# Kernel tuning notes

Hardware: AMD Instinct MI355X
Metric: run time of the kernel (lower is better)

The kernel has to match this reference:

```python
import jax, jax.numpy as jnp
import numpy as np

VOCAB = 50257
EMBED = 512
HIDDEN = 1024
UNITS = HIDDEN // 2  # per-direction LSTM units
B, S, T = 32, 8, 128


def _lstm_bias(units):
    # Keras unit_forget_bias=True: bias = [0 (i), 1 (f), 0 (c), 0 (o)]
    return jnp.concatenate([jnp.zeros((units,)), jnp.ones((units,)),
                            jnp.zeros((2 * units,))])


def setup_inputs() -> dict:
    key = jax.random.key(0)
    ks = jax.random.split(key, 8)
    # token ids with variable-length zero padding (pad_token_id=0)
    x = jax.random.randint(ks[0], (B, S, T), 1, VOCAB)
    lengths = jax.random.randint(ks[1], (B, S, 1), T // 2, T + 1)
    pos = jnp.arange(T)[None, None, :]
    x = jnp.where(pos < lengths, x, 0).astype(jnp.int32)

    emb_table = jax.random.normal(ks[2], (VOCAB, EMBED), jnp.float32) * 0.05

    def glorot(k, shape):
        fan = np.sqrt(2.0 / (shape[0] + shape[1]))
        return jax.random.normal(k, shape, jnp.float32) * fan

    W_f = glorot(ks[3], (EMBED, 4 * UNITS))
    U_f = glorot(ks[4], (UNITS, 4 * UNITS))
    W_b = glorot(ks[5], (EMBED, 4 * UNITS))
    U_b = glorot(ks[6], (UNITS, 4 * UNITS))
    b_f = _lstm_bias(UNITS)
    b_b = _lstm_bias(UNITS)
    return {"x": x, "emb_table": emb_table,
            "W_f": W_f, "U_f": U_f, "b_f": b_f,
            "W_b": W_b, "U_b": U_b, "b_b": b_b}


def _masked_lstm_final(xW, mask, U):
    """xW: (N, T, 4u) precomputed input projections (+bias); mask: (N, T) bool.
    Returns final hidden state (N, u) with Keras masking semantics: masked
    timesteps are skipped (state held)."""
    N = xW.shape[0]
    u = U.shape[0]
    h0 = jnp.zeros((N, u), xW.dtype)
    c0 = jnp.zeros((N, u), xW.dtype)

    def step(carry, inp):
        h, c = carry
        z, m = inp  # z: (N, 4u), m: (N,)
        z = z + h @ U
        i, f, g, o = jnp.split(z, 4, axis=-1)
        i = jax.nn.sigmoid(i)
        f = jax.nn.sigmoid(f)
        g = jnp.tanh(g)
        o = jax.nn.sigmoid(o)
        c_new = f * c + i * g
        h_new = o * jnp.tanh(c_new)
        m = m[:, None]
        return (jnp.where(m, h_new, h), jnp.where(m, c_new, c)), None

    (hT, _), _ = jax.lax.scan(
        step, (h0, c0),
        (jnp.swapaxes(xW, 0, 1), jnp.swapaxes(mask, 0, 1)))
    return hT


def reference(x, emb_table, W_f, U_f, b_f, W_b, U_b, b_b):
    Bx, Sx, Tx = x.shape
    N = Bx * Sx
    ids = x.reshape(N, Tx)
    mask = ids != 0  # mask_zero=True
    emb = emb_table[ids]  # (N, T, E)

    # forward direction
    xWf = emb @ W_f + b_f  # (N, T, 4u), one big GEMM up front
    h_fwd = _masked_lstm_final(xWf, mask, U_f)

    # backward direction: reverse time and mask (Keras go_backwards)
    emb_rev = emb[:, ::-1, :]
    mask_rev = mask[:, ::-1]
    xWb = emb_rev @ W_b + b_b
    h_bwd = _masked_lstm_final(xWb, mask_rev, U_b)

    out = jnp.concatenate([h_fwd, h_bwd], axis=-1)  # (N, hidden_dim)
    return out.reshape(Bx, Sx, HIDDEN)
```

## Files before the change

kernel.cpp:

```cpp
#include <hip/hip_runtime.h>

typedef _Float16 half_t;
typedef _Float16 half8 __attribute__((ext_vector_type(8)));
typedef float floatx4 __attribute__((ext_vector_type(4)));

#define NSEQ   256
#define TLEN   128
#define EMBD   512
#define UNITSZ 512
#define GC     2048
#define NTOK   32768
#define NCOL   4096
#define KDIM   512

constexpr size_t OFF_EMB = 0;
constexpr size_t OFF_WT  = 33554432;
constexpr size_t OFF_UT  = OFF_WT + 4194304;
constexpr size_t OFF_HB  = OFF_UT + 4194304;
constexpr size_t OFF_CNT = OFF_HB + 1048576;
constexpr size_t OFF_MSK = OFF_CNT + 4096;
constexpr size_t OFF_XW  = OFF_MSK + 4096;

__device__ inline float sigm(float x)  { return 1.0f / (1.0f + __expf(-x)); }
__device__ inline float tanhx(float x) { return 2.0f / (1.0f + __expf(-2.0f * x)) - 1.0f; }

__device__ inline unsigned long long ld8c(const void* p) {
    return __hip_atomic_load((const unsigned long long*)p, __ATOMIC_RELAXED, __HIP_MEMORY_SCOPE_AGENT);
}
__device__ inline void st8c(void* p, unsigned long long v) {
    __hip_atomic_store((unsigned long long*)p, v, __ATOMIC_RELAXED, __HIP_MEMORY_SCOPE_AGENT);
}

__global__ void pack_kernel(const float* __restrict__ Wf, const float* __restrict__ Uf,
                            const float* __restrict__ Wb, const float* __restrict__ Ub,
                            half_t* __restrict__ WT, half_t* __restrict__ UT) {
    int c = blockIdx.x * 256 + threadIdx.x;
    int arr = c >> 18;
    int r = c & 262143;
    int kc = r >> 12;
    int gc = r & 4095;
    int dir = gc >> 11;
    int g = gc & 2047;
    const float* src = (arr == 0) ? (dir ? Wb : Wf) : (dir ? Ub : Uf);
    half_t* dst = (arr == 0) ? WT : UT;
    half8 v;
#pragma unroll
    for (int j = 0; j < 8; ++j)
        v[j] = (half_t)src[(size_t)(kc * 8 + j) * GC + g];
    *(half8*)(dst + (size_t)gc * KDIM + kc * 8) = v;
}

__global__ void zero_kernel(unsigned* __restrict__ hb_and_cnt) {
    int i = blockIdx.x * 256 + threadIdx.x;
    if (i < 263168) hb_and_cnt[i] = 0u;
}

__global__ void mask_kernel(const int* __restrict__ x, unsigned long long* __restrict__ mk) {
    int n = blockIdx.x;
    int l = threadIdx.x;
    unsigned long long b0 = __ballot(x[n * TLEN + l] != 0);
    unsigned long long b1 = __ballot(x[n * TLEN + 64 + l] != 0);
    if (l == 0) { mk[n * 2] = b0; mk[n * 2 + 1] = b1; }
}

__global__ void gather_kernel(const int* __restrict__ x, const float* __restrict__ tab,
                              half_t* __restrict__ embf) {
    int g = blockIdx.x * 256 + threadIdx.x;
    int token = g >> 6;
    int k = (g & 63) * 8;
    int id = x[token];
    const float* s = tab + (size_t)id * EMBD + k;
    float4 a = *(const float4*)(s);
    float4 b = *(const float4*)(s + 4);
    half8 v;
    v[0] = (half_t)a.x; v[1] = (half_t)a.y; v[2] = (half_t)a.z; v[3] = (half_t)a.w;
    v[4] = (half_t)b.x; v[5] = (half_t)b.y; v[6] = (half_t)b.z; v[7] = (half_t)b.w;
    *(half8*)(embf + (size_t)token * EMBD + k) = v;
}

__global__ __launch_bounds__(256, 2) void gemm_kernel(const half_t* __restrict__ embf,
                                                      const half_t* __restrict__ WT,
                                                      const float* __restrict__ bf,
                                                      const float* __restrict__ bb,
                                                      half_t* __restrict__ xw) {
    __shared__ half_t As[128 * 40];
    __shared__ half_t Bs[128 * 40];
    int bx = blockIdx.x;
    int bm = bx & 255, bn = bx >> 8;
    int r0 = bm * 128, c0 = bn * 128;
    int tid = threadIdx.x;
    int w = tid >> 6, l = tid & 63;
    int q = l >> 4, cl = l & 15;
    int mq = (w >> 1) * 64, nq = (w & 1) * 64;

    floatx4 acc[4][4];
#pragma unroll
    for (int a = 0; a < 4; ++a)
#pragma unroll
        for (int b = 0; b < 4; ++b) acc[a][b] = (floatx4){0.f, 0.f, 0.f, 0.f};

    for (int kb = 0; kb < 16; ++kb) {
#pragma unroll
        for (int cc = 0; cc < 2; ++cc) {
            int c = tid + cc * 256;
            int row = c >> 2, qt = c & 3;
            half8 va = *(const half8*)(embf + (size_t)(r0 + row) * KDIM + kb * 32 + qt * 8);
            *(half8*)(As + row * 40 + qt * 8) = va;
            half8 vb = *(const half8*)(WT + (size_t)(c0 + row) * KDIM + kb * 32 + qt * 8);
            *(half8*)(Bs + row * 40 + qt * 8) = vb;
        }
        __syncthreads();
        half8 af[4], bfr[4];
#pragma unroll
        for (int mb = 0; mb < 4; ++mb)
            af[mb] = *(const half8*)(As + (mq + mb * 16 + cl) * 40 + q * 8);
#pragma unroll
        for (int nb = 0; nb < 4; ++nb)
            bfr[nb] = *(const half8*)(Bs + (nq + nb * 16 + cl) * 40 + q * 8);
#pragma unroll
        for (int mb = 0; mb < 4; ++mb)
#pragma unroll
            for (int nb = 0; nb < 4; ++nb)
                acc[mb][nb] = __builtin_amdgcn_mfma_f32_16x16x32_f16(af[mb], bfr[nb], acc[mb][nb], 0, 0, 0);
        __syncthreads();
    }
#pragma unroll
    for (int nb = 0; nb < 4; ++nb) {
        int col = c0 + nq + nb * 16 + cl;
        int dir = col >> 11, gcol = col & 2047;
        float bias = dir ? bb[gcol] : bf[gcol];
#pragma unroll
        for (int mb = 0; mb < 4; ++mb) {
#pragma unroll
            for (int r = 0; r < 4; ++r) {
                int row = r0 + mq + mb * 16 + q * 4 + r;
                xw[(size_t)row * NCOL + col] = (half_t)(acc[mb][nb][r] + bias);
            }
        }
    }
}

__global__ __launch_bounds__(256, 1) void lstm_kernel(const half_t* __restrict__ xw,
                                                      const half_t* __restrict__ UT,
                                                      half_t* __restrict__ hbuf,
                                                      const unsigned long long* __restrict__ mk,
                                                      float* __restrict__ out,
                                                      unsigned* __restrict__ cnt) {
    __shared__ half_t Ast[8192];
    __shared__ half_t Pk[1024];
    int bx = blockIdx.x;
    int dir = bx >> 7;
    int rowg = (bx >> 3) & 15;
    int wgc = bx & 7;
    int tid = threadIdx.x;
    int w = tid >> 6, l = tid & 63;
    int q = l >> 4, cl = l & 15;
    int cg = wgc * 4 + w;
    int ub = cg * 16;
    int ub0 = wgc * 64;
    int r0 = rowg * 16;

    half8 bfrag[64];
#pragma unroll
    for (int kk = 0; kk < 16; ++kk)
#pragma unroll
        for (int cf = 0; cf < 4; ++cf)
            bfrag[kk * 4 + cf] = *(const half8*)(UT + (size_t)(dir * 2048 + cf * 512 + ub + cl) * KDIM + kk * 32 + q * 8);

    unsigned long long mlo[4], mhi[4];
#pragma unroll
    for (int r = 0; r < 4; ++r) {
        int n = r0 + q * 4 + r;
        mlo[r] = mk[n * 2];
        mhi[r] = mk[n * 2 + 1];
    }

    float cs[4] = {0.f, 0.f, 0.f, 0.f};
    float hs[4] = {0.f, 0.f, 0.f, 0.f};
    unsigned* cptr = cnt + (dir * 16 + rowg) * 16;
    int colb = dir * 2048 + ub + cl;

    half_t xv[4][4];
    {
        int tIdx = dir ? 127 : 0;
#pragma unroll
        for (int r = 0; r < 4; ++r) {
            size_t ro = ((size_t)(r0 + q * 4 + r) * TLEN + tIdx) * NCOL;
#pragma unroll
            for (int g = 0; g < 4; ++g)
                xv[g][r] = xw[ro + colb + g * 512];
        }
    }

#pragma unroll 1
    for (int t = 0; t < TLEN; ++t) {
        int tIdx = dir ? (127 - t) : t;
        int rpar = t & 1, wpar = rpar ^ 1;
        if (t > 0) {
            if (tid == 0) {
                while (__hip_atomic_load(cptr, __ATOMIC_RELAXED, __HIP_MEMORY_SCOPE_AGENT) < (unsigned)(32 * t))
                    __builtin_amdgcn_s_sleep(1);
            }
            __syncthreads();
        }
        const half_t* hsrc = hbuf + (size_t)(dir * 2 + rpar) * NSEQ * UNITSZ;
#pragma unroll
        for (int cc = 0; cc < 4; ++cc) {
            int c = tid + cc * 256;
            int kk = c >> 6, ll = c & 63;
            int m = ll & 15, koff = kk * 32 + (ll >> 4) * 8;
            const half_t* sp = hsrc + (size_t)(r0 + m) * UNITSZ + koff;
            union { unsigned long long u[2]; half8 v; } cv;
            cv.u[0] = ld8c(sp);
            cv.u[1] = ld8c(sp + 4);
            *(half8*)(Ast + c * 8) = cv.v;
        }
        __syncthreads();
        floatx4 a0, a1, a2, a3;
#pragma unroll
        for (int r = 0; r < 4; ++r) {
            a0[r] = (float)xv[0][r];
            a1[r] = (float)xv[1][r];
            a2[r] = (float)xv[2][r];
            a3[r] = (float)xv[3][r];
        }
#pragma unroll
        for (int kk = 0; kk < 16; ++kk) {
            half8 af = *(const half8*)(Ast + (kk * 64 + l) * 8);
            a0 = __builtin_amdgcn_mfma_f32_16x16x32_f16(af, bfrag[kk * 4 + 0], a0, 0, 0, 0);
            a1 = __builtin_amdgcn_mfma_f32_16x16x32_f16(af, bfrag[kk * 4 + 1], a1, 0, 0, 0);
            a2 = __builtin_amdgcn_mfma_f32_16x16x32_f16(af, bfrag[kk * 4 + 2], a2, 0, 0, 0);
            a3 = __builtin_amdgcn_mfma_f32_16x16x32_f16(af, bfrag[kk * 4 + 3], a3, 0, 0, 0);
        }
#pragma unroll
        for (int r = 0; r < 4; ++r) {
            unsigned long long mw = (tIdx & 64) ? mhi[r] : mlo[r];
            bool keep = (mw >> (tIdx & 63)) & 1ull;
            float iv = sigm(a0[r]);
            float fv = sigm(a1[r]);
            float gv = tanhx(a2[r]);
            float ov = sigm(a3[r]);
            float cn = fv * cs[r] + iv * gv;
            float hn = ov * tanhx(cn);
            if (keep) { cs[r] = cn; hs[r] = hn; }
            Pk[(q * 4 + r) * 64 + w * 16 + cl] = (half_t)hs[r];
        }
        __syncthreads();
        half_t* hdst = hbuf + (size_t)(dir * 2 + wpar) * NSEQ * UNITSZ;
        {
            int prow = tid >> 4, pch = tid & 15;
            unsigned long long pv = *(const unsigned long long*)(Pk + prow * 64 + pch * 4);
            st8c(hdst + (size_t)(r0 + prow) * UNITSZ + ub0 + pch * 4, pv);
        }
        asm volatile("" ::: "memory");
        if (t + 1 < TLEN) {
            int tN = dir ? (126 - t) : (t + 1);
#pragma unroll
            for (int r = 0; r < 4; ++r) {
                size_t ro = ((size_t)(r0 + q * 4 + r) * TLEN + tN) * NCOL;
#pragma unroll
                for (int g = 0; g < 4; ++g)
                    xv[g][r] = xw[ro + colb + g * 512];
            }
        }
        asm volatile("s_waitcnt vmcnt(16)" ::: "memory");
        if (l == 0)
            __hip_atomic_fetch_add(cptr, 1u, __ATOMIC_RELAXED, __HIP_MEMORY_SCOPE_AGENT);
    }
#pragma unroll
    for (int r = 0; r < 4; ++r) {
        int n = r0 + q * 4 + r;
        out[(size_t)n * 1024 + dir * 512 + ub + cl] = hs[r];
    }
}

extern "C" void kernel_launch(void* const* d_in, const int* in_sizes, int n_in,
                              void* d_out, int out_size, void* d_ws, size_t ws_size,
                              hipStream_t stream) {
    const int*   x    = (const int*)d_in[0];
    const float* tab  = (const float*)d_in[1];
    const float* Wf   = (const float*)d_in[2];
    const float* Uf   = (const float*)d_in[3];
    const float* bf   = (const float*)d_in[4];
    const float* Wb   = (const float*)d_in[5];
    const float* Ub   = (const float*)d_in[6];
    const float* bb   = (const float*)d_in[7];
    float* out = (float*)d_out;

    char* ws = (char*)d_ws;
    half_t*   embf = (half_t*)(ws + OFF_EMB);
    half_t*   WT   = (half_t*)(ws + OFF_WT);
    half_t*   UT   = (half_t*)(ws + OFF_UT);
    half_t*   hbuf = (half_t*)(ws + OFF_HB);
    unsigned* cnt  = (unsigned*)(ws + OFF_CNT);
    unsigned long long* mkb = (unsigned long long*)(ws + OFF_MSK);
    half_t*   xw   = (half_t*)(ws + OFF_XW);
    unsigned* hbz  = (unsigned*)(ws + OFF_HB);

    pack_kernel<<<2048, 256, 0, stream>>>(Wf, Uf, Wb, Ub, WT, UT);
    zero_kernel<<<1028, 256, 0, stream>>>(hbz);
    mask_kernel<<<256, 64, 0, stream>>>(x, mkb);
    gather_kernel<<<8192, 256, 0, stream>>>(x, tab, embf);
    gemm_kernel<<<8192, 256, 0, stream>>>(embf, WT, bf, bb, xw);
    lstm_kernel<<<256, 256, 0, stream>>>(xw, UT, hbuf, mkb, out, cnt);
}
```

Measured before the change: 1.108 ms.

## Interleave two 8-row LSTM chains per workgroup and use per-WG flag sync

```diff
diff --git a/kernel.cpp b/kernel.cpp
--- a/kernel.cpp
+++ b/kernel.cpp
@@ -29,6 +29,12 @@
 }
 __device__ inline void st8c(void* p, unsigned long long v) {
     __hip_atomic_store((unsigned long long*)p, v, __ATOMIC_RELAXED, __HIP_MEMORY_SCOPE_AGENT);
+}
+__device__ inline unsigned ld4c(const void* p) {
+    return __hip_atomic_load((const unsigned*)p, __ATOMIC_RELAXED, __HIP_MEMORY_SCOPE_AGENT);
+}
+__device__ inline void st4c(void* p, unsigned v) {
+    __hip_atomic_store((unsigned*)p, v, __ATOMIC_RELAXED, __HIP_MEMORY_SCOPE_AGENT);
 }
 
 __global__ void pack_kernel(const float* __restrict__ Wf, const float* __restrict__ Uf,
@@ -147,10 +153,10 @@
                                                       float* __restrict__ out,
                                                       unsigned* __restrict__ cnt) {
     __shared__ half_t Ast[8192];
-    __shared__ half_t Pk[1024];
+    __shared__ half_t Pk[512];
     int bx = blockIdx.x;
     int dir = bx >> 7;
-    int rowg = (bx >> 3) & 15;
+    int p = (bx >> 3) & 15;
     int wgc = bx & 7;
     int tid = threadIdx.x;
     int w = tid >> 6, l = tid & 63;
@@ -158,7 +164,8 @@
     int cg = wgc * 4 + w;
     int ub = cg * 16;
     int ub0 = wgc * 64;
-    int r0 = rowg * 16;
+    bool val = (q < 2);
+    int rowg[2] = {p, p + 16};
 
     half8 bfrag[64];
 #pragma unroll
@@ -167,110 +174,137 @@
         for (int cf = 0; cf < 4; ++cf)
             bfrag[kk * 4 + cf] = *(const half8*)(UT + (size_t)(dir * 2048 + cf * 512 + ub + cl) * KDIM + kk * 32 + q * 8);
 
-    unsigned long long mlo[4], mhi[4];
-#pragma unroll
-    for (int r = 0; r < 4; ++r) {
-        int n = r0 + q * 4 + r;
-        mlo[r] = mk[n * 2];
-        mhi[r] = mk[n * 2 + 1];
-    }
-
-    float cs[4] = {0.f, 0.f, 0.f, 0.f};
-    float hs[4] = {0.f, 0.f, 0.f, 0.f};
-    unsigned* cptr = cnt + (dir * 16 + rowg) * 16;
+    unsigned long long mlo[2][4], mhi[2][4];
+#pragma unroll
+    for (int ph = 0; ph < 2; ++ph)
+#pragma unroll
+        for (int r = 0; r < 4; ++r) {
+            int n = rowg[ph] * 8 + (q & 1) * 4 + r;
+            mlo[ph][r] = mk[n * 2];
+            mhi[ph][r] = mk[n * 2 + 1];
+        }
+
+    float cs[2][4] = {{0.f,0.f,0.f,0.f},{0.f,0.f,0.f,0.f}};
+    float hs[2][4] = {{0.f,0.f,0.f,0.f},{0.f,0.f,0.f,0.f}};
     int colb = dir * 2048 + ub + cl;
 
-    half_t xv[4][4];
-    {
-        int tIdx = dir ? 127 : 0;
+    half_t xv[2][16];
+    if (val) {
+        int tI = dir ? 127 : 0;
 #pragma unroll
         for (int r = 0; r < 4; ++r) {
-            size_t ro = ((size_t)(r0 + q * 4 + r) * TLEN + tIdx) * NCOL;
+            size_t ro = ((size_t)(rowg[0] * 8 + q * 4 + r) * TLEN + tI) * NCOL;
 #pragma unroll
             for (int g = 0; g < 4; ++g)
-                xv[g][r] = xw[ro + colb + g * 512];
-        }
-    }
+                xv[0][g * 4 + r] = xw[ro + colb + g * 512];
+        }
+    }
+
+#pragma unroll
+    for (int cc = 0; cc < 2; ++cc) {
+        int c = tid + cc * 256;
+        int kk = c >> 5, j = c & 31;
+        int qd = j >> 3, mm = 8 + (j & 7);
+        half8 z = {(half_t)0,(half_t)0,(half_t)0,(half_t)0,(half_t)0,(half_t)0,(half_t)0,(half_t)0};
+        *(half8*)(Ast + (kk * 64 + qd * 16 + mm) * 8) = z;
+    }
+    __syncthreads();
 
 #pragma unroll 1
     for (int t = 0; t < TLEN; ++t) {
-        int tIdx = dir ? (127 - t) : t;
-        int rpar = t & 1, wpar = rpar ^ 1;
-        if (t > 0) {
-            if (tid == 0) {
-                while (__hip_atomic_load(cptr, __ATOMIC_RELAXED, __HIP_MEMORY_SCOPE_AGENT) < (unsigned)(32 * t))
+#pragma unroll
+        for (int ph = 0; ph < 2; ++ph) {
+            int rg = rowg[ph];
+            int chain = dir * 32 + rg;
+            unsigned* sq = cnt + chain * 16;
+            if (w == 0) {
+                for (;;) {
+                    unsigned v = ld4c(sq + (l & 7));
+                    if (!__ballot(v < (unsigned)t)) break;
                     __builtin_amdgcn_s_sleep(1);
+                }
             }
             __syncthreads();
-        }
-        const half_t* hsrc = hbuf + (size_t)(dir * 2 + rpar) * NSEQ * UNITSZ;
-#pragma unroll
-        for (int cc = 0; cc < 4; ++cc) {
-            int c = tid + cc * 256;
-            int kk = c >> 6, ll = c & 63;
-            int m = ll & 15, koff = kk * 32 + (ll >> 4) * 8;
-            const half_t* sp = hsrc + (size_t)(r0 + m) * UNITSZ + koff;
-            union { unsigned long long u[2]; half8 v; } cv;
-            cv.u[0] = ld8c(sp);
-            cv.u[1] = ld8c(sp + 4);
-            *(half8*)(Ast + c * 8) = cv.v;
-        }
-        __syncthreads();
-        floatx4 a0, a1, a2, a3;
-#pragma unroll
-        for (int r = 0; r < 4; ++r) {
-            a0[r] = (float)xv[0][r];
-            a1[r] = (float)xv[1][r];
-            a2[r] = (float)xv[2][r];
-            a3[r] = (float)xv[3][r];
-        }
-#pragma unroll
-        for (int kk = 0; kk < 16; ++kk) {
-            half8 af = *(const half8*)(Ast + (kk * 64 + l) * 8);
-            a0 = __builtin_amdgcn_mfma_f32_16x16x32_f16(af, bfrag[kk * 4 + 0], a0, 0, 0, 0);
-            a1 = __builtin_amdgcn_mfma_f32_16x16x32_f16(af, bfrag[kk * 4 + 1], a1, 0, 0, 0);
-            a2 = __builtin_amdgcn_mfma_f32_16x16x32_f16(af, bfrag[kk * 4 + 2], a2, 0, 0, 0);
-            a3 = __builtin_amdgcn_mfma_f32_16x16x32_f16(af, bfrag[kk * 4 + 3], a3, 0, 0, 0);
-        }
-#pragma unroll
-        for (int r = 0; r < 4; ++r) {
-            unsigned long long mw = (tIdx & 64) ? mhi[r] : mlo[r];
-            bool keep = (mw >> (tIdx & 63)) & 1ull;
-            float iv = sigm(a0[r]);
-            float fv = sigm(a1[r]);
-            float gv = tanhx(a2[r]);
-            float ov = sigm(a3[r]);
-            float cn = fv * cs[r] + iv * gv;
-            float hn = ov * tanhx(cn);
-            if (keep) { cs[r] = cn; hs[r] = hn; }
-            Pk[(q * 4 + r) * 64 + w * 16 + cl] = (half_t)hs[r];
-        }
-        __syncthreads();
-        half_t* hdst = hbuf + (size_t)(dir * 2 + wpar) * NSEQ * UNITSZ;
-        {
-            int prow = tid >> 4, pch = tid & 15;
-            unsigned long long pv = *(const unsigned long long*)(Pk + prow * 64 + pch * 4);
-            st8c(hdst + (size_t)(r0 + prow) * UNITSZ + ub0 + pch * 4, pv);
-        }
-        asm volatile("" ::: "memory");
-        if (t + 1 < TLEN) {
-            int tN = dir ? (126 - t) : (t + 1);
+            const half_t* hsrc = hbuf + (((size_t)chain * 2 + (t & 1)) * 8) * UNITSZ;
+#pragma unroll
+            for (int cc = 0; cc < 2; ++cc) {
+                int c = tid + cc * 256;
+                int kk = c >> 5, j = c & 31;
+                int qd = j >> 3, m = j & 7;
+                int koff = kk * 32 + qd * 8;
+                const half_t* sp = hsrc + (size_t)m * UNITSZ + koff;
+                union { unsigned long long u[2]; half8 v; } cv;
+                cv.u[0] = ld8c(sp);
+                cv.u[1] = ld8c(sp + 4);
+                *(half8*)(Ast + (kk * 64 + qd * 16 + m) * 8) = cv.v;
+            }
+            __syncthreads();
+            floatx4 a0, a1, a2, a3;
 #pragma unroll
             for (int r = 0; r < 4; ++r) {
-                size_t ro = ((size_t)(r0 + q * 4 + r) * TLEN + tN) * NCOL;
-#pragma unroll
-                for (int g = 0; g < 4; ++g)
-                    xv[g][r] = xw[ro + colb + g * 512];
-            }
-        }
-        asm volatile("s_waitcnt vmcnt(16)" ::: "memory");
-        if (l == 0)
-            __hip_atomic_fetch_add(cptr, 1u, __ATOMIC_RELAXED, __HIP_MEMORY_SCOPE_AGENT);
-    }
-#pragma unroll
-    for (int r = 0; r < 4; ++r) {
-        int n = r0 + q * 4 + r;
-        out[(size_t)n * 1024 + dir * 512 + ub + cl] = hs[r];
+                a0[r] = val ? (float)xv[ph][0 * 4 + r] : 0.f;
+                a1[r] = val ? (float)xv[ph][1 * 4 + r] : 0.f;
+                a2[r] = val ? (float)xv[ph][2 * 4 + r] : 0.f;
+                a3[r] = val ? (float)xv[ph][3 * 4 + r] : 0.f;
+            }
+#pragma unroll
+            for (int kk = 0; kk < 16; ++kk) {
+                half8 af = *(const half8*)(Ast + (kk * 64 + l) * 8);
+                a0 = __builtin_amdgcn_mfma_f32_16x16x32_f16(af, bfrag[kk * 4 + 0], a0, 0, 0, 0);
+                a1 = __builtin_amdgcn_mfma_f32_16x16x32_f16(af, bfrag[kk * 4 + 1], a1, 0, 0, 0);
+                a2 = __builtin_amdgcn_mfma_f32_16x16x32_f16(af, bfrag[kk * 4 + 2], a2, 0, 0, 0);
+                a3 = __builtin_amdgcn_mfma_f32_16x16x32_f16(af, bfrag[kk * 4 + 3], a3, 0, 0, 0);
+            }
+            int tIdx = dir ? (127 - t) : t;
+            if (val) {
+#pragma unroll
+                for (int r = 0; r < 4; ++r) {
+                    unsigned long long mw = (tIdx & 64) ? mhi[ph][r] : mlo[ph][r];
+                    bool keep = (mw >> (tIdx & 63)) & 1ull;
+                    float iv = sigm(a0[r]);
+                    float fv = sigm(a1[r]);
+                    float gv = tanhx(a2[r]);
+                    float ov = sigm(a3[r]);
+                    float cn = fv * cs[ph][r] + iv * gv;
+                    float hn = ov * tanhx(cn);
+                    if (keep) { cs[ph][r] = cn; hs[ph][r] = hn; }
+                    Pk[(q * 4 + r) * 64 + w * 16 + cl] = (half_t)hs[ph][r];
+                }
+            }
+            __syncthreads();
+            half_t* hdst = hbuf + (((size_t)chain * 2 + ((t + 1) & 1)) * 8) * UNITSZ;
+            if (w == 0) {
+                int prow = l >> 3, pu = (l & 7) * 8;
+                const unsigned long long* ps = (const unsigned long long*)(Pk + prow * 64 + pu);
+                st8c(hdst + (size_t)prow * UNITSZ + ub0 + pu, ps[0]);
+                st8c(hdst + (size_t)prow * UNITSZ + ub0 + pu + 4, ps[1]);
+            }
+            asm volatile("" ::: "memory");
+            int nph = ph ^ 1;
+            int ntv = (ph == 0) ? t : t + 1;
+            if (ntv < TLEN && val) {
+                int tN = dir ? (127 - ntv) : ntv;
+                int nrg = rowg[nph];
+#pragma unroll
+                for (int r = 0; r < 4; ++r) {
+                    size_t ro = ((size_t)(nrg * 8 + q * 4 + r) * TLEN + tN) * NCOL;
+#pragma unroll
+                    for (int g = 0; g < 4; ++g)
+                        xv[nph][g * 4 + r] = xw[ro + colb + g * 512];
+                }
+            }
+            asm volatile("s_waitcnt vmcnt(16)" ::: "memory");
+            if (tid == 0) st4c(sq + wgc, (unsigned)(t + 1));
+        }
+    }
+    if (val) {
+#pragma unroll
+        for (int ph = 0; ph < 2; ++ph)
+#pragma unroll
+            for (int r = 0; r < 4; ++r) {
+                int n = rowg[ph] * 8 + q * 4 + r;
+                out[(size_t)n * 1024 + dir * 512 + ub + cl] = hs[ph][r];
+            }
     }
 }
 
```

Measured after the change: 1.292 ms. 16.6% more time.
